# Kernel tuning notes

Hardware: AMD Instinct MI355X
Metric: run time of the kernel (lower is better)

The kernel has to match this reference:

```python
import jax, jax.numpy as jnp
import numpy as np

C = 256
CQK = C // 8


def setup_inputs() -> dict:
    key = jax.random.key(0)
    ks = jax.random.split(key, 8)
    B, H, W = 4, 64, 64
    x = jax.random.normal(ks[0], (B, C, H, W), dtype=jnp.float32)
    # 1x1 conv weights are plain [out_c, in_c] matrices + bias
    sq = 1.0 / np.sqrt(C)
    Wq = jax.random.uniform(ks[1], (CQK, C), jnp.float32, -sq, sq)
    bq = jax.random.uniform(ks[2], (CQK,), jnp.float32, -sq, sq)
    Wk = jax.random.uniform(ks[3], (CQK, C), jnp.float32, -sq, sq)
    bk = jax.random.uniform(ks[4], (CQK,), jnp.float32, -sq, sq)
    Wv = jax.random.uniform(ks[5], (C, C), jnp.float32, -sq, sq)
    bv = jax.random.uniform(ks[6], (C,), jnp.float32, -sq, sq)
    gamma = jnp.zeros((1,), dtype=jnp.float32)
    return {"x": x, "Wq": Wq, "bq": bq, "Wk": Wk, "bk": bk, "Wv": Wv, "bv": bv, "gamma": gamma}


def reference(x, Wq, bq, Wk, bk, Wv, bv, gamma):
    B, Cc, H, W = x.shape
    N = H * W
    xf = x.reshape(B, Cc, N)  # [B, C, N]
    # 1x1 convs == channel GEMMs
    q = jnp.einsum('dc,bcn->bdn', Wq, xf) + bq[None, :, None]  # [B, C/8, N]
    k = jnp.einsum('dc,bcn->bdn', Wk, xf) + bk[None, :, None]  # [B, C/8, N]
    v = jnp.einsum('dc,bcn->bdn', Wv, xf) + bv[None, :, None]  # [B, C, N]
    # attention[b, i, j] = softmax_j( q_i . k_j )  (no scaling, as in source)
    attn = jax.nn.softmax(jnp.einsum('bdn,bdm->bnm', q, k), axis=-1)  # [B, N, N]
    # out = value @ attention  (note: NOT attention^T, faithful to source)
    out = jnp.einsum('bcn,bnm->bcm', v, attn)  # [B, C, N]
    out = out.reshape(B, Cc, H, W)
    return gamma[0] * out + x
```

## Files before the change

### kernel.cpp

```cpp
#include <hip/hip_runtime.h>
#include <hip/hip_bf16.h>


#define NB 4
#define CC 256
#define NN 4096
#define L2E 1.44269504088896340f

typedef short  short4v  __attribute__((ext_vector_type(4)));
typedef short  short8v  __attribute__((ext_vector_type(8)));
typedef __bf16 bf16x8   __attribute__((ext_vector_type(8)));
typedef float  f32x4    __attribute__((ext_vector_type(4)));
typedef float  f32x16   __attribute__((ext_vector_type(16)));
typedef unsigned long u64x2 __attribute__((ext_vector_type(2)));
typedef unsigned int u32;

#define AS1 __attribute__((address_space(1)))
#define AS3 __attribute__((address_space(3)))

static __device__ __forceinline__ void gload16(const void* g, void* l) {
  __builtin_amdgcn_global_load_lds((const AS1 u32*)g, (AS3 u32*)l, 16, 0, 0);
}

static __device__ __forceinline__ unsigned short f2bf(float f) {
  union { __bf16 h; unsigned short u; } v; v.h = (__bf16)f; return v.u;
}
static __device__ __forceinline__ float bf2f(unsigned short u) {
  union { unsigned u; float f; } v; v.u = (u32)u << 16; return v.f;
}

union FragU { short8v s; bf16x8 b; unsigned u[4]; };

static __device__ __forceinline__ bf16x8 ld_frag(const unsigned short* p) {
  FragU u; u.s = *(const short8v*)p; return u.b;
}

static __device__ __forceinline__ f32x16 zero16() {
  f32x16 v;
#pragma unroll
  for (int i = 0; i < 16; ++i) v[i] = 0.0f;
  return v;
}

static __device__ __forceinline__ f32x16 mfma32(bf16x8 a, bf16x8 b, f32x16 c) {
  return __builtin_amdgcn_mfma_f32_32x32x16_bf16(a, b, c, 0, 0, 0);
}

__global__ __launch_bounds__(256) void k_wcvt(
    const float* __restrict__ Wq, const float* __restrict__ Wk,
    const float* __restrict__ Wv, unsigned short* __restrict__ Wb)
{
  const int i4 = blockIdx.x * 256 + threadIdx.x;
  const int e = i4 * 4;
  const int row = e >> 8, c = e & 255;
  const float* src = (row < 32) ? (Wq + row * 256 + c)
                   : (row < 64) ? (Wk + (row - 32) * 256 + c)
                                : (Wv + (row - 64) * 256 + c);
  f32x4 v = *(const f32x4*)src;
  short4v s;
#pragma unroll
  for (int j = 0; j < 4; ++j) s[j] = (short)f2bf(v[j]);
  *(short4v*)(Wb + e) = s;
}

__global__ __launch_bounds__(256) void k_proj(
    const float* __restrict__ x, const unsigned short* __restrict__ Wb,
    const float* __restrict__ bq, const float* __restrict__ bk,
    const float* __restrict__ bv,
    unsigned short* __restrict__ Qt, unsigned short* __restrict__ Kt,
    unsigned char* __restrict__ V8)
{
  __shared__ unsigned short xs[32][268];
  const int t = threadIdx.x;
  const int b = blockIdx.y;
  const int n0 = blockIdx.x * 32;
  const int w = t >> 6, l = t & 63, h = l >> 5, col = l & 31;

  const float* xb = x + (size_t)b * CC * NN;
  {
    const int c_off = t >> 3, nl = 4 * (t & 7);
#pragma unroll
    for (int c0 = 0; c0 < CC; c0 += 32) {
      int c = c0 + c_off;
      f32x4 v4 = *(const f32x4*)(xb + (size_t)c * NN + n0 + nl);
#pragma unroll
      for (int j = 0; j < 4; ++j) xs[nl + j][c] = f2bf(v4[j]);
    }
  }
  __syncthreads();

  for (int f = w; f < 10; f += 4) {
    const float* bsrc; int rowbase; int mode; int wrow;
    if (f == 0)      { bsrc = bq; rowbase = 0;            mode = 0; wrow = 0; }
    else if (f == 1) { bsrc = bk; rowbase = 0;            mode = 1; wrow = 32; }
    else             { bsrc = bv; rowbase = (f - 2) * 32; mode = 2; wrow = 64 + rowbase; }

    f32x16 acc0 = zero16();
    const unsigned short* wr = Wb + (size_t)(wrow + col) * 256 + 8 * h;

#pragma unroll
    for (int k0 = 0; k0 < CC; k0 += 16) {
      FragU a;
      a.s = *(const short8v*)(wr + k0);
      const unsigned short* p0 = &xs[col][k0 + 8 * h];
      FragU b0;
      short4v t0a = *(const short4v*)p0, t0b = *(const short4v*)(p0 + 4);
#pragma unroll
      for (int j = 0; j < 4; ++j) { b0.s[j] = t0a[j]; b0.s[4 + j] = t0b[j]; }
      acc0 = mfma32(a.b, b0.b, acc0);
    }

    const int n = n0 + col;
#pragma unroll
    for (int q = 0; q < 4; ++q) {
      f32x4 bias4 = *(const f32x4*)(bsrc + rowbase + 8 * q + 4 * h);
      float vals[4];
#pragma unroll
      for (int i = 0; i < 4; ++i) vals[i] = acc0[4 * q + i] + bias4[i];
      if (mode == 2) {
        const size_t tb = ((((size_t)b * 128 + (n >> 5)) * 2 + ((n >> 3) & 1)) * 256) * 16
                          + ((n >> 4) & 1) * 8 + (n & 7);
        u32 w01 = __builtin_amdgcn_cvt_pk_fp8_f32(vals[0], vals[1], 0, false);
        u32 w23 = __builtin_amdgcn_cvt_pk_fp8_f32(vals[2], vals[3], 0, false);
        const int cb0 = rowbase + 8 * q + 4 * h;
        V8[tb + (size_t)(cb0 + 0) * 16] = (unsigned char)(w01 & 0xff);
        V8[tb + (size_t)(cb0 + 1) * 16] = (unsigned char)((w01 >> 8) & 0xff);
        V8[tb + (size_t)(cb0 + 2) * 16] = (unsigned char)(w23 & 0xff);
        V8[tb + (size_t)(cb0 + 3) * 16] = (unsigned char)((w23 >> 8) & 0xff);
      } else {
        unsigned short* dst = (mode == 0) ? Qt : Kt;
        const float scale = (mode == 0) ? L2E : 1.0f;
        short4v s4;
#pragma unroll
        for (int i = 0; i < 4; ++i) s4[i] = (short)f2bf(vals[i] * scale);
        *(short4v*)(dst + ((size_t)b * NN + n) * 32 + 8 * q + 4 * h) = s4;
      }
    }
  }
}

__global__ __launch_bounds__(512) void k_rowstats(
    const unsigned short* __restrict__ Qt, const unsigned short* __restrict__ Kt,
    float* __restrict__ cbias)
{
  __shared__ float ssum[8][64];
  const int t = threadIdx.x;
  const int w = t >> 6, l = t & 63, h = l >> 5, col = l & 31;
  const int b = blockIdx.y;
  const int n0 = blockIdx.x * 64;
  const unsigned short* Qb = Qt + (size_t)b * NN * 32;
  const unsigned short* Kb = Kt + (size_t)b * NN * 32;

  bf16x8 bq00 = ld_frag(Qb + (size_t)(n0 + col) * 32 + 8 * h);
  bf16x8 bq01 = ld_frag(Qb + (size_t)(n0 + col) * 32 + 16 + 8 * h);
  bf16x8 bq10 = ld_frag(Qb + (size_t)(n0 + 32 + col) * 32 + 8 * h);
  bf16x8 bq11 = ld_frag(Qb + (size_t)(n0 + 32 + col) * 32 + 16 + 8 * h);

  float acc0 = 0.0f, acc1 = 0.0f;
  const int mbase = w * (NN / 8);
#pragma unroll 2
  for (int mt = 0; mt < 16; ++mt) {
    const int m0 = mbase + mt * 32;
    bf16x8 ak0 = ld_frag(Kb + (size_t)(m0 + col) * 32 + 8 * h);
    bf16x8 ak1 = ld_frag(Kb + (size_t)(m0 + col) * 32 + 16 + 8 * h);
    f32x16 S0 = zero16(), S1 = zero16();
    S0 = mfma32(ak0, bq00, S0);
    S0 = mfma32(ak1, bq01, S0);
    S1 = mfma32(ak0, bq10, S1);
    S1 = mfma32(ak1, bq11, S1);
    float p0 = 0.0f, p1 = 0.0f, p2 = 0.0f, p3 = 0.0f;
#pragma unroll
    for (int r = 0; r < 8; ++r) {
      p0 += __builtin_amdgcn_exp2f(S0[r]);
      p1 += __builtin_amdgcn_exp2f(S0[8 + r]);
      p2 += __builtin_amdgcn_exp2f(S1[r]);
      p3 += __builtin_amdgcn_exp2f(S1[8 + r]);
    }
    acc0 += p0 + p1;
    acc1 += p2 + p3;
  }
  acc0 += __shfl_xor(acc0, 32);
  acc1 += __shfl_xor(acc1, 32);

  if (l < 32) { ssum[w][l] = acc0; ssum[w][32 + l] = acc1; }
  __syncthreads();

  if (t < 64) {
    float s = 0.0f;
#pragma unroll
    for (int wv = 0; wv < 8; ++wv) s += ssum[wv][t];
    cbias[(size_t)b * NN + n0 + t] = -__builtin_amdgcn_logf(s);
  }
}

#define V_ISSUE(SET, TJ)                                                       \
  {                                                                            \
    const char* vg_ = vg + (size_t)(TJ) * 8192;                                \
    SET##A0 = *(const u64x2*)(vg_);                                            \
    SET##B0 = *(const u64x2*)(vg_ + 512);                                      \
    SET##A1 = *(const u64x2*)(vg_ + 8192);                                     \
    SET##B1 = *(const u64x2*)(vg_ + 8192 + 512);                               \
  }

#define PV_U(EBP, vA, vB)                                                      \
  {                                                                            \
    const char* eb_ = (EBP);                                                   \
    u64x2 ev0 = *(const u64x2*)(eb_);                                          \
    u64x2 ev1 = *(const u64x2*)(eb_ + 1024);                                   \
    u64x2 ev2 = *(const u64x2*)(eb_ + 2048);                                   \
    u64x2 ev3 = *(const u64x2*)(eb_ + 3072);                                   \
    long v00 = (long)vA[0], v10 = (long)vA[1];                                 \
    long v01 = (long)vB[0], v11 = (long)vB[1];                                 \
    acc[0][0] = __builtin_amdgcn_mfma_f32_32x32x16_fp8_fp8((long)ev0[0], v00, acc[0][0], 0, 0, 0); \
    acc[1][0] = __builtin_amdgcn_mfma_f32_32x32x16_fp8_fp8((long)ev1[0], v00, acc[1][0], 0, 0, 0); \
    acc[2][0] = __builtin_amdgcn_mfma_f32_32x32x16_fp8_fp8((long)ev2[0], v00, acc[2][0], 0, 0, 0); \
    acc[3][0] = __builtin_amdgcn_mfma_f32_32x32x16_fp8_fp8((long)ev3[0], v00, acc[3][0], 0, 0, 0); \
    acc[0][1] = __builtin_amdgcn_mfma_f32_32x32x16_fp8_fp8((long)ev0[0], v01, acc[0][1], 0, 0, 0); \
    acc[1][1] = __builtin_amdgcn_mfma_f32_32x32x16_fp8_fp8((long)ev1[0], v01, acc[1][1], 0, 0, 0); \
    acc[2][1] = __builtin_amdgcn_mfma_f32_32x32x16_fp8_fp8((long)ev2[0], v01, acc[2][1], 0, 0, 0); \
    acc[3][1] = __builtin_amdgcn_mfma_f32_32x32x16_fp8_fp8((long)ev3[0], v01, acc[3][1], 0, 0, 0); \
    acc[0][0] = __builtin_amdgcn_mfma_f32_32x32x16_fp8_fp8((long)ev0[1], v10, acc[0][0], 0, 0, 0); \
    acc[1][0] = __builtin_amdgcn_mfma_f32_32x32x16_fp8_fp8((long)ev1[1], v10, acc[1][0], 0, 0, 0); \
    acc[2][0] = __builtin_amdgcn_mfma_f32_32x32x16_fp8_fp8((long)ev2[1], v10, acc[2][0], 0, 0, 0); \
    acc[3][0] = __builtin_amdgcn_mfma_f32_32x32x16_fp8_fp8((long)ev3[1], v10, acc[3][0], 0, 0, 0); \
    acc[0][1] = __builtin_amdgcn_mfma_f32_32x32x16_fp8_fp8((long)ev0[1], v11, acc[0][1], 0, 0, 0); \
    acc[1][1] = __builtin_amdgcn_mfma_f32_32x32x16_fp8_fp8((long)ev1[1], v11, acc[1][1], 0, 0, 0); \
    acc[2][1] = __builtin_amdgcn_mfma_f32_32x32x16_fp8_fp8((long)ev2[1], v11, acc[2][1], 0, 0, 0); \
    acc[3][1] = __builtin_amdgcn_mfma_f32_32x32x16_fp8_fp8((long)ev3[1], v11, acc[3][1], 0, 0, 0); \
  }

#define K3_ITER(J, CUR, NXT)                                                   \
  if ((J) <= KJ) {                                                             \
    const int j_ = (J);                                                        \
    if (j_ + 1 < KJ) {                                                         \
      const size_t qoff_ = (size_t)(2 * j_ + 2) * 2048;                        \
      const int qs_ = (j_ + 1) & 1;                                            \
      if (ll == l) {                                                           \
        gload16(qsrc + qoff_, &qbuf[qs_][0][w * 256]);                         \
        gload16(qsrc + qoff_ + 2048, &qbuf[qs_][1][w * 256]);                  \
      }                                                                        \
    }                                                                          \
    if (w < 4) {                                                               \
      if (j_ < KJ) {                                                           \
        _Pragma("unroll")                                                      \
        for (int u = 0; u < 2; ++u) {                                          \
          const char* qb = &qbuf[j_ & 1][u][0];                                \
          FragU fq0, fq1;                                                      \
          fq0.s = *(const short8v*)(qb + l * 16);                              \
          fq1.s = *(const short8v*)(qb + 1024 + l * 16);                       \
          f32x16 S = zero16();                                                 \
          S = mfma32(fq0.b, bk0, S);                                           \
          S = mfma32(fq1.b, bk1, S);                                           \
          float e[16];                                                         \
          const float* cbi = cb + (2 * j_ + u) * 32;                           \
          _Pragma("unroll")                                                    \
          for (int q = 0; q < 4; ++q) {                                        \
            f32x4 cb4 = *(const f32x4*)(cbi + 8 * q + 4 * h);                  \
            _Pragma("unroll")                                                  \
            for (int i = 0; i < 4; ++i)                                        \
              e[4 * q + i] = __builtin_amdgcn_exp2f(S[4 * q + i] + cb4[i]);    \
          }                                                                    \
          u32 wA = __builtin_amdgcn_cvt_pk_fp8_f32(e[0], e[1], 0, false);      \
          wA = __builtin_amdgcn_cvt_pk_fp8_f32(e[2], e[3], wA, true);          \
          u32 wB = __builtin_amdgcn_cvt_pk_fp8_f32(e[4], e[5], 0, false);      \
          wB = __builtin_amdgcn_cvt_pk_fp8_f32(e[6], e[7], wB, true);          \
          u32 wC = __builtin_amdgcn_cvt_pk_fp8_f32(e[8], e[9], 0, false);      \
          wC = __builtin_amdgcn_cvt_pk_fp8_f32(e[10], e[11], wC, true);        \
          u32 wD = __builtin_amdgcn_cvt_pk_fp8_f32(e[12], e[13], 0, false);    \
          wD = __builtin_amdgcn_cvt_pk_fp8_f32(e[14], e[15], wD, true);        \
          asm("v_permlane32_swap_b32 %0, %1" : "+v"(wA), "+v"(wB));            \
          asm("v_permlane32_swap_b32 %0, %1" : "+v"(wC), "+v"(wD));            \
          u64x2 ev;                                                            \
          ev[0] = ((unsigned long)wB << 32) | wA;                              \
          ev[1] = ((unsigned long)wD << 32) | wC;                              \
          *(u64x2*)(&ebuf[j_ & 1][u][mfp * 1024 + l * 16]) = ev;               \
        }                                                                      \
      }                                                                        \
    } else {                                                                   \
      if (j_ < KJ) V_ISSUE(NXT, 2 * j_)                                        \
      if (j_ > 0) {                                                            \
        __builtin_amdgcn_s_setprio(1);                                         \
        PV_U(&ebuf[(j_ - 1) & 1][0][l * 16], CUR##A0, CUR##B0)                 \
        PV_U(&ebuf[(j_ - 1) & 1][1][l * 16], CUR##A1, CUR##B1)                 \
        __builtin_amdgcn_s_setprio(0);                                         \
      }                                                                        \
    }                                                                          \
    if (j_ < KJ) __syncthreads();                                              \
  }

__global__ __launch_bounds__(512) void k_attn_out(
    const unsigned short* __restrict__ Qt, const unsigned short* __restrict__ Kt,
    const unsigned char* __restrict__ V8,
    const float* __restrict__ cbias,
    unsigned short* __restrict__ pout,
    int nsplit, int nlen)
{
  __shared__ __align__(16) char qbuf[2][2][2048];
  __shared__ __align__(16) char ebuf[2][2][4096];

  const int wg = (int)blockIdx.x;
  const int chunk = (int)gridDim.x >> 3;
  const int id2 = (wg & 7) * chunk + (wg >> 3);
  const int per_b = 32 * nsplit;
  const int b = id2 / per_b;
  const int rem = id2 - b * per_b;
  const int ns = rem >> 5;
  const int m0 = (rem & 31) * 128;
  const int nbeg = ns * nlen;

  const int t = threadIdx.x;
  const int w = t >> 6, l = t & 63, h = l >> 5, col = l & 31;
  const int mfp = w & 3;
  const int ccons = (w & 3) * 64;

  const unsigned short* Kb = Kt + (size_t)b * NN * 32;
  const float* cb = cbias + (size_t)b * NN + nbeg;

  bf16x8 bk0 = ld_frag(Kb + (size_t)(m0 + 32 * mfp + col) * 32 + 8 * h);
  bf16x8 bk1 = ld_frag(Kb + (size_t)(m0 + 32 * mfp + col) * 32 + 16 + 8 * h);

  const int ll = l & 15;
  const size_t gqoff = (size_t)(((w & 1) * 16 + ll) * 64 + ((w >> 1) & 1) * 16
                                + (w >> 2) * 32);
  const char* qsrc = (const char*)Qt + ((size_t)b * NN + nbeg) * 64 + gqoff;

  const char* vg = (const char*)V8
      + (((size_t)b * 128 + (nbeg >> 5)) * 2 + h) * 4096
      + (size_t)(ccons + col) * 16;

  f32x16 acc[4][2];
#pragma unroll
  for (int mf = 0; mf < 4; ++mf)
#pragma unroll
    for (int cf = 0; cf < 2; ++cf) acc[mf][cf] = zero16();

  u64x2 S0A0, S0B0, S0A1, S0B1;
  u64x2 S1A0, S1B0, S1A1, S1B1;
  S0A0 = S0B0 = S0A1 = S0B1 = (u64x2)0;
  S1A0 = S1B0 = S1A1 = S1B1 = (u64x2)0;

  const int KJ = nlen >> 6;

  if (ll == l) {
    gload16(qsrc, &qbuf[0][0][w * 256]);
    gload16(qsrc + 2048, &qbuf[0][1][w * 256]);
  }
  __syncthreads();

  for (int jj = 0; jj <= KJ; jj += 2) {
    K3_ITER(jj,     S0, S1)
    K3_ITER(jj + 1, S1, S0)
  }

  if (w >= 4) {
    unsigned short* pb = pout + (((size_t)ns * NB + b) * NN + m0) * CC + ccons;
#pragma unroll
    for (int mf = 0; mf < 4; ++mf)
#pragma unroll
      for (int cf = 0; cf < 2; ++cf)
#pragma unroll
        for (int r = 0; r < 16; ++r) {
          int mloc = 32 * mf + (r & 3) + 8 * (r >> 2) + 4 * h;
          pb[(size_t)mloc * CC + 32 * cf + col] = f2bf(acc[mf][cf][r]);
        }
  }
}

__global__ __launch_bounds__(256) void k_comb(
    const unsigned short* __restrict__ pout, const float* __restrict__ x,
    const float* __restrict__ gamma, float* __restrict__ out, int nsplit)
{
  __shared__ float ld[64][65];
  const size_t STRIDE = (size_t)NB * CC * NN;
  const int t = threadIdx.x;
  const int m0 = blockIdx.x * 64, c0 = blockIdx.y * 64, b = blockIdx.z;
  const int ci = t & 63, mo = t >> 6;

  const unsigned short* pb = pout + ((size_t)b * NN + m0) * CC + c0;
#pragma unroll
  for (int rep = 0; rep < 16; ++rep) {
    const int mi = 4 * rep + mo;
    float s = bf2f(pb[(size_t)mi * CC + ci]);
    for (int ns = 1; ns < nsplit; ++ns)
      s += bf2f(pb[ns * STRIDE + (size_t)mi * CC + ci]);
    ld[mi][ci] = s;
  }
  __syncthreads();

  const float g = gamma[0];
  const int mi2 = t & 63;
#pragma unroll
  for (int rep = 0; rep < 16; ++rep) {
    const int cj = 4 * rep + mo;
    const size_t idx = ((size_t)b * CC + c0 + cj) * NN + m0 + mi2;
    out[idx] = g * ld[mi2][cj] + x[idx];
  }
}

extern "C" void kernel_launch(void* const* d_in, const int* in_sizes, int n_in,
                              void* d_out, int out_size, void* d_ws, size_t ws_size,
                              hipStream_t stream) {
  const float* x     = (const float*)d_in[0];
  const float* Wq    = (const float*)d_in[1];
  const float* bq    = (const float*)d_in[2];
  const float* Wk    = (const float*)d_in[3];
  const float* bk    = (const float*)d_in[4];
  const float* Wv    = (const float*)d_in[5];
  const float* bv    = (const float*)d_in[6];
  const float* gamma = (const float*)d_in[7];
  float* out = (float*)d_out;

  char* ws = (char*)d_ws;
  unsigned short* Qt = (unsigned short*)(ws);
  unsigned short* Kt = (unsigned short*)(ws + (1u << 20));
  unsigned char*  V8 = (unsigned char*)(ws + (2u << 20));
  unsigned short* Wb = (unsigned short*)(ws + (6u << 20));
  float* cbias = (float*)(ws + (10u << 20) + (2u << 18));
  const size_t POUT_OFF = (11u << 20);
  unsigned short* pout = (unsigned short*)(ws + POUT_OFF);
  const size_t PART_BYTES = (size_t)NB * CC * NN * 2;

  int nsplit = (ws_size >= POUT_OFF + 2 * PART_BYTES) ? 2 : 1;

  k_wcvt<<<dim3(80), 256, 0, stream>>>(Wq, Wk, Wv, Wb);
  k_proj<<<dim3(NN / 32, NB), 256, 0, stream>>>(x, Wb, bq, bk, bv, Qt, Kt, V8);
  k_rowstats<<<dim3(NN / 64, NB), 512, 0, stream>>>(Qt, Kt, cbias);
  k_attn_out<<<dim3(128 * nsplit), 512, 0, stream>>>(
      Qt, Kt, V8, cbias, pout, nsplit, NN / nsplit);
  k_comb<<<dim3(NN / 64, CC / 64, NB), 256, 0, stream>>>(pout, x, gamma, out, nsplit);
}
```

Baseline: 94.42 us.

## Replace producer/consumer wave split with uniform waves doing both QK and PV

The attention-output kernel previously split its 8 waves into 4 producers (QK^T, exp, fp8 pack into LDS) and 4 consumers (V loads plus PV MFMAs). Now every wave computes one 32x32 score tile and exp-packs it, then runs PV on 32 output channels with half the accumulators. Work is spread evenly and interleaved within each wave, so the exp/VALU phase and the MFMA phase can overlap across all waves instead of leaving half the waves idle in each phase. The cost is that each wave now loads twice as many E fragments from LDS per unit of PV work and holds both the QK and PV register state.

```diff
diff --git a/kernel.cpp b/kernel.cpp
--- a/kernel.cpp
+++ b/kernel.cpp
@@ -196,94 +196,96 @@
 #define V_ISSUE(SET, TJ)                                                       \
   {                                                                            \
     const char* vg_ = vg + (size_t)(TJ) * 8192;                                \
-    SET##A0 = *(const u64x2*)(vg_);                                            \
-    SET##B0 = *(const u64x2*)(vg_ + 512);                                      \
-    SET##A1 = *(const u64x2*)(vg_ + 8192);                                     \
-    SET##B1 = *(const u64x2*)(vg_ + 8192 + 512);                               \
-  }
-
-#define PV_U(EBP, vA, vB)                                                      \
+    SET##A = *(const u64x2*)(vg_);                                             \
+    SET##B = *(const u64x2*)(vg_ + 8192);                                      \
+  }
+
+#define PV_INT(EBSEL, vA, vB)                                                  \
   {                                                                            \
-    const char* eb_ = (EBP);                                                   \
-    u64x2 ev0 = *(const u64x2*)(eb_);                                          \
-    u64x2 ev1 = *(const u64x2*)(eb_ + 1024);                                   \
-    u64x2 ev2 = *(const u64x2*)(eb_ + 2048);                                   \
-    u64x2 ev3 = *(const u64x2*)(eb_ + 3072);                                   \
-    long v00 = (long)vA[0], v10 = (long)vA[1];                                 \
-    long v01 = (long)vB[0], v11 = (long)vB[1];                                 \
-    acc[0][0] = __builtin_amdgcn_mfma_f32_32x32x16_fp8_fp8((long)ev0[0], v00, acc[0][0], 0, 0, 0); \
-    acc[1][0] = __builtin_amdgcn_mfma_f32_32x32x16_fp8_fp8((long)ev1[0], v00, acc[1][0], 0, 0, 0); \
-    acc[2][0] = __builtin_amdgcn_mfma_f32_32x32x16_fp8_fp8((long)ev2[0], v00, acc[2][0], 0, 0, 0); \
-    acc[3][0] = __builtin_amdgcn_mfma_f32_32x32x16_fp8_fp8((long)ev3[0], v00, acc[3][0], 0, 0, 0); \
-    acc[0][1] = __builtin_amdgcn_mfma_f32_32x32x16_fp8_fp8((long)ev0[0], v01, acc[0][1], 0, 0, 0); \
-    acc[1][1] = __builtin_amdgcn_mfma_f32_32x32x16_fp8_fp8((long)ev1[0], v01, acc[1][1], 0, 0, 0); \
-    acc[2][1] = __builtin_amdgcn_mfma_f32_32x32x16_fp8_fp8((long)ev2[0], v01, acc[2][1], 0, 0, 0); \
-    acc[3][1] = __builtin_amdgcn_mfma_f32_32x32x16_fp8_fp8((long)ev3[0], v01, acc[3][1], 0, 0, 0); \
-    acc[0][0] = __builtin_amdgcn_mfma_f32_32x32x16_fp8_fp8((long)ev0[1], v10, acc[0][0], 0, 0, 0); \
-    acc[1][0] = __builtin_amdgcn_mfma_f32_32x32x16_fp8_fp8((long)ev1[1], v10, acc[1][0], 0, 0, 0); \
-    acc[2][0] = __builtin_amdgcn_mfma_f32_32x32x16_fp8_fp8((long)ev2[1], v10, acc[2][0], 0, 0, 0); \
-    acc[3][0] = __builtin_amdgcn_mfma_f32_32x32x16_fp8_fp8((long)ev3[1], v10, acc[3][0], 0, 0, 0); \
-    acc[0][1] = __builtin_amdgcn_mfma_f32_32x32x16_fp8_fp8((long)ev0[1], v11, acc[0][1], 0, 0, 0); \
-    acc[1][1] = __builtin_amdgcn_mfma_f32_32x32x16_fp8_fp8((long)ev1[1], v11, acc[1][1], 0, 0, 0); \
-    acc[2][1] = __builtin_amdgcn_mfma_f32_32x32x16_fp8_fp8((long)ev2[1], v11, acc[2][1], 0, 0, 0); \
-    acc[3][1] = __builtin_amdgcn_mfma_f32_32x32x16_fp8_fp8((long)ev3[1], v11, acc[3][1], 0, 0, 0); \
+    const char* eb0_ = &ebuf[EBSEL][0][l * 16];                                \
+    const char* eb1_ = &ebuf[EBSEL][1][l * 16];                                \
+    u64x2 e00 = *(const u64x2*)(eb0_);                                         \
+    u64x2 e01 = *(const u64x2*)(eb0_ + 1024);                                  \
+    u64x2 e02 = *(const u64x2*)(eb0_ + 2048);                                  \
+    u64x2 e03 = *(const u64x2*)(eb0_ + 3072);                                  \
+    u64x2 e10 = *(const u64x2*)(eb1_);                                         \
+    u64x2 e11 = *(const u64x2*)(eb1_ + 1024);                                  \
+    u64x2 e12 = *(const u64x2*)(eb1_ + 2048);                                  \
+    u64x2 e13 = *(const u64x2*)(eb1_ + 3072);                                  \
+    long va0 = (long)vA[0], va1 = (long)vA[1];                                 \
+    long vb0 = (long)vB[0], vb1 = (long)vB[1];                                 \
+    acc[0] = __builtin_amdgcn_mfma_f32_32x32x16_fp8_fp8((long)e00[0], va0, acc[0], 0, 0, 0); \
+    acc[1] = __builtin_amdgcn_mfma_f32_32x32x16_fp8_fp8((long)e01[0], va0, acc[1], 0, 0, 0); \
+    acc[2] = __builtin_amdgcn_mfma_f32_32x32x16_fp8_fp8((long)e02[0], va0, acc[2], 0, 0, 0); \
+    acc[3] = __builtin_amdgcn_mfma_f32_32x32x16_fp8_fp8((long)e03[0], va0, acc[3], 0, 0, 0); \
+    acc[0] = __builtin_amdgcn_mfma_f32_32x32x16_fp8_fp8((long)e00[1], va1, acc[0], 0, 0, 0); \
+    acc[1] = __builtin_amdgcn_mfma_f32_32x32x16_fp8_fp8((long)e01[1], va1, acc[1], 0, 0, 0); \
+    acc[2] = __builtin_amdgcn_mfma_f32_32x32x16_fp8_fp8((long)e02[1], va1, acc[2], 0, 0, 0); \
+    acc[3] = __builtin_amdgcn_mfma_f32_32x32x16_fp8_fp8((long)e03[1], va1, acc[3], 0, 0, 0); \
+    acc[0] = __builtin_amdgcn_mfma_f32_32x32x16_fp8_fp8((long)e10[0], vb0, acc[0], 0, 0, 0); \
+    acc[1] = __builtin_amdgcn_mfma_f32_32x32x16_fp8_fp8((long)e11[0], vb0, acc[1], 0, 0, 0); \
+    acc[2] = __builtin_amdgcn_mfma_f32_32x32x16_fp8_fp8((long)e12[0], vb0, acc[2], 0, 0, 0); \
+    acc[3] = __builtin_amdgcn_mfma_f32_32x32x16_fp8_fp8((long)e13[0], vb0, acc[3], 0, 0, 0); \
+    acc[0] = __builtin_amdgcn_mfma_f32_32x32x16_fp8_fp8((long)e10[1], vb1, acc[0], 0, 0, 0); \
+    acc[1] = __builtin_amdgcn_mfma_f32_32x32x16_fp8_fp8((long)e11[1], vb1, acc[1], 0, 0, 0); \
+    acc[2] = __builtin_amdgcn_mfma_f32_32x32x16_fp8_fp8((long)e12[1], vb1, acc[2], 0, 0, 0); \
+    acc[3] = __builtin_amdgcn_mfma_f32_32x32x16_fp8_fp8((long)e13[1], vb1, acc[3], 0, 0, 0); \
   }
 
 #define K3_ITER(J, CUR, NXT)                                                   \
   if ((J) <= KJ) {                                                             \
     const int j_ = (J);                                                        \
-    if (j_ + 1 < KJ) {                                                         \
+                                                             \
+    if (j_ + 1 < KJ && ll == l) {                                              \
       const size_t qoff_ = (size_t)(2 * j_ + 2) * 2048;                        \
       const int qs_ = (j_ + 1) & 1;                                            \
-      if (ll == l) {                                                           \
-        gload16(qsrc + qoff_, &qbuf[qs_][0][w * 256]);                         \
-        gload16(qsrc + qoff_ + 2048, &qbuf[qs_][1][w * 256]);                  \
+      gload16(qsrc + qoff_, &qbuf[qs_][0][w * 256]);                           \
+      gload16(qsrc + qoff_ + 2048, &qbuf[qs_][1][w * 256]);                    \
+    }                                                                          \
+                         \
+    if (j_ < KJ) V_ISSUE(NXT, 2 * j_)                                          \
+                                           \
+    f32x16 S;                                                                  \
+    if (j_ < KJ) {                                                             \
+      const char* qb = &qbuf[j_ & 1][up][0];                                   \
+      FragU fq0, fq1;                                                          \
+      fq0.s = *(const short8v*)(qb + l * 16);                                  \
+      fq1.s = *(const short8v*)(qb + 1024 + l * 16);                           \
+      S = zero16();                                                            \
+      S = mfma32(fq0.b, bk0, S);                                               \
+      S = mfma32(fq1.b, bk1, S);                                               \
+    }                                                                          \
+                                 \
+    if (j_ > 0) {                                                              \
+      __builtin_amdgcn_s_setprio(1);                                          \
+      PV_INT((j_ - 1) & 1, CUR##A, CUR##B)                                     \
+      __builtin_amdgcn_s_setprio(0);                                          \
+    }                                                                          \
+                                                       \
+    if (j_ < KJ) {                                                             \
+      float e[16];                                                             \
+      const float* cbi = cb + (2 * j_ + up) * 32;                              \
+      _Pragma("unroll")                                                        \
+      for (int q = 0; q < 4; ++q) {                                            \
+        f32x4 cb4 = *(const f32x4*)(cbi + 8 * q + 4 * h);                      \
+        _Pragma("unroll")                                                      \
+        for (int i = 0; i < 4; ++i)                                            \
+          e[4 * q + i] = __builtin_amdgcn_exp2f(S[4 * q + i] + cb4[i]);        \
       }                                                                        \
-    }                                                                          \
-    if (w < 4) {                                                               \
-      if (j_ < KJ) {                                                           \
-        _Pragma("unroll")                                                      \
-        for (int u = 0; u < 2; ++u) {                                          \
-          const char* qb = &qbuf[j_ & 1][u][0];                                \
-          FragU fq0, fq1;                                                      \
-          fq0.s = *(const short8v*)(qb + l * 16);                              \
-          fq1.s = *(const short8v*)(qb + 1024 + l * 16);                       \
-          f32x16 S = zero16();                                                 \
-          S = mfma32(fq0.b, bk0, S);                                           \
-          S = mfma32(fq1.b, bk1, S);                                           \
-          float e[16];                                                         \
-          const float* cbi = cb + (2 * j_ + u) * 32;                           \
-          _Pragma("unroll")                                                    \
-          for (int q = 0; q < 4; ++q) {                                        \
-            f32x4 cb4 = *(const f32x4*)(cbi + 8 * q + 4 * h);                  \
-            _Pragma("unroll")                                                  \
-            for (int i = 0; i < 4; ++i)                                        \
-              e[4 * q + i] = __builtin_amdgcn_exp2f(S[4 * q + i] + cb4[i]);    \
-          }                                                                    \
-          u32 wA = __builtin_amdgcn_cvt_pk_fp8_f32(e[0], e[1], 0, false);      \
-          wA = __builtin_amdgcn_cvt_pk_fp8_f32(e[2], e[3], wA, true);          \
-          u32 wB = __builtin_amdgcn_cvt_pk_fp8_f32(e[4], e[5], 0, false);      \
-          wB = __builtin_amdgcn_cvt_pk_fp8_f32(e[6], e[7], wB, true);          \
-          u32 wC = __builtin_amdgcn_cvt_pk_fp8_f32(e[8], e[9], 0, false);      \
-          wC = __builtin_amdgcn_cvt_pk_fp8_f32(e[10], e[11], wC, true);        \
-          u32 wD = __builtin_amdgcn_cvt_pk_fp8_f32(e[12], e[13], 0, false);    \
-          wD = __builtin_amdgcn_cvt_pk_fp8_f32(e[14], e[15], wD, true);        \
-          asm("v_permlane32_swap_b32 %0, %1" : "+v"(wA), "+v"(wB));            \
-          asm("v_permlane32_swap_b32 %0, %1" : "+v"(wC), "+v"(wD));            \
-          u64x2 ev;                                                            \
-          ev[0] = ((unsigned long)wB << 32) | wA;                              \
-          ev[1] = ((unsigned long)wD << 32) | wC;                              \
-          *(u64x2*)(&ebuf[j_ & 1][u][mfp * 1024 + l * 16]) = ev;               \
-        }                                                                      \
-      }                                                                        \
-    } else {                                                                   \
-      if (j_ < KJ) V_ISSUE(NXT, 2 * j_)                                        \
-      if (j_ > 0) {                                                            \
-        __builtin_amdgcn_s_setprio(1);                                         \
-        PV_U(&ebuf[(j_ - 1) & 1][0][l * 16], CUR##A0, CUR##B0)                 \
-        PV_U(&ebuf[(j_ - 1) & 1][1][l * 16], CUR##A1, CUR##B1)                 \
-        __builtin_amdgcn_s_setprio(0);                                         \
-      }                                                                        \
+      u32 wA = __builtin_amdgcn_cvt_pk_fp8_f32(e[0], e[1], 0, false);          \
+      wA = __builtin_amdgcn_cvt_pk_fp8_f32(e[2], e[3], wA, true);              \
+      u32 wB = __builtin_amdgcn_cvt_pk_fp8_f32(e[4], e[5], 0, false);          \
+      wB = __builtin_amdgcn_cvt_pk_fp8_f32(e[6], e[7], wB, true);              \
+      u32 wC = __builtin_amdgcn_cvt_pk_fp8_f32(e[8], e[9], 0, false);          \
+      wC = __builtin_amdgcn_cvt_pk_fp8_f32(e[10], e[11], wC, true);            \
+      u32 wD = __builtin_amdgcn_cvt_pk_fp8_f32(e[12], e[13], 0, false);        \
+      wD = __builtin_amdgcn_cvt_pk_fp8_f32(e[14], e[15], wD, true);            \
+      asm("v_permlane32_swap_b32 %0, %1" : "+v"(wA), "+v"(wB));                \
+      asm("v_permlane32_swap_b32 %0, %1" : "+v"(wC), "+v"(wD));                \
+      u64x2 ev;                                                                \
+      ev[0] = ((unsigned long)wB << 32) | wA;                                  \
+      ev[1] = ((unsigned long)wD << 32) | wC;                                  \
+      *(u64x2*)(&ebuf[j_ & 1][up][mfp * 1024 + l * 16]) = ev;                  \
     }                                                                          \
     if (j_ < KJ) __syncthreads();                                              \
   }
@@ -310,8 +312,9 @@
 
   const int t = threadIdx.x;
   const int w = t >> 6, l = t & 63, h = l >> 5, col = l & 31;
-  const int mfp = w & 3;
-  const int ccons = (w & 3) * 64;
+  const int up = w & 1;
+  const int mfp = w >> 1;
+  const int ccons = w * 32;
 
   const unsigned short* Kb = Kt + (size_t)b * NN * 32;
   const float* cb = cbias + (size_t)b * NN + nbeg;
@@ -328,16 +331,12 @@
       + (((size_t)b * 128 + (nbeg >> 5)) * 2 + h) * 4096
       + (size_t)(ccons + col) * 16;
 
-  f32x16 acc[4][2];
-#pragma unroll
-  for (int mf = 0; mf < 4; ++mf)
-#pragma unroll
-    for (int cf = 0; cf < 2; ++cf) acc[mf][cf] = zero16();
-
-  u64x2 S0A0, S0B0, S0A1, S0B1;
-  u64x2 S1A0, S1B0, S1A1, S1B1;
-  S0A0 = S0B0 = S0A1 = S0B1 = (u64x2)0;
-  S1A0 = S1B0 = S1A1 = S1B1 = (u64x2)0;
+  f32x16 acc[4];
+#pragma unroll
+  for (int mf = 0; mf < 4; ++mf) acc[mf] = zero16();
+
+  u64x2 S0A, S0B, S1A, S1B;
+  S0A = S0B = S1A = S1B = (u64x2)0;
 
   const int KJ = nlen >> 6;
 
@@ -352,17 +351,15 @@
     K3_ITER(jj + 1, S1, S0)
   }
 
-  if (w >= 4) {
+  {
     unsigned short* pb = pout + (((size_t)ns * NB + b) * NN + m0) * CC + ccons;
 #pragma unroll
     for (int mf = 0; mf < 4; ++mf)
 #pragma unroll
-      for (int cf = 0; cf < 2; ++cf)
-#pragma unroll
-        for (int r = 0; r < 16; ++r) {
-          int mloc = 32 * mf + (r & 3) + 8 * (r >> 2) + 4 * h;
-          pb[(size_t)mloc * CC + 32 * cf + col] = f2bf(acc[mf][cf][r]);
-        }
+      for (int r = 0; r < 16; ++r) {
+        int mloc = 32 * mf + (r & 3) + 8 * (r >> 2) + 4 * h;
+        pb[(size_t)mloc * CC + col] = f2bf(acc[mf][r]);
+      }
   }
 }
 
```

Result: slower. 98.07 us (+3.9%).

## Materialize fp8 attention matrix in global memory, split into emat and PV kernels

Applied to the files above, without the earlier changes.

Replaces the fused attention-output kernel, which recomputed exponentials in LDS with producer/consumer warps and split-N partial outputs, with two kernels. The first writes the full fp8 exp-matrix E to global memory, and the second runs the PV GEMM and fuses the gamma*out + x epilogue, so the partial-sum combine kernel goes away. The aim is simpler, fully parallel stages without intra-block syncs or split reductions. In exchange it writes and reads a 64MB fp8 matrix (4x4096x4096 bytes) through HBM, which adds substantial memory traffic.

```diff
diff --git a/kernel.cpp b/kernel.cpp
--- a/kernel.cpp
+++ b/kernel.cpp
@@ -15,13 +15,6 @@
 typedef unsigned long u64x2 __attribute__((ext_vector_type(2)));
 typedef unsigned int u32;
 
-#define AS1 __attribute__((address_space(1)))
-#define AS3 __attribute__((address_space(3)))
-
-static __device__ __forceinline__ void gload16(const void* g, void* l) {
-  __builtin_amdgcn_global_load_lds((const AS1 u32*)g, (AS3 u32*)l, 16, 0, 0);
-}
-
 static __device__ __forceinline__ unsigned short f2bf(float f) {
   union { __bf16 h; unsigned short u; } v; v.h = (__bf16)f; return v.u;
 }
@@ -44,6 +37,9 @@
 
 static __device__ __forceinline__ f32x16 mfma32(bf16x8 a, bf16x8 b, f32x16 c) {
   return __builtin_amdgcn_mfma_f32_32x32x16_bf16(a, b, c, 0, 0, 0);
+}
+static __device__ __forceinline__ f32x16 mfma8(long a, long b, f32x16 c) {
+  return __builtin_amdgcn_mfma_f32_32x32x16_fp8_fp8(a, b, c, 0, 0, 0);
 }
 
 __global__ __launch_bounds__(256) void k_wcvt(
@@ -193,207 +189,117 @@
   }
 }
 
-#define V_ISSUE(SET, TJ)                                                       \
-  {                                                                            \
-    const char* vg_ = vg + (size_t)(TJ) * 8192;                                \
-    SET##A0 = *(const u64x2*)(vg_);                                            \
-    SET##B0 = *(const u64x2*)(vg_ + 512);                                      \
-    SET##A1 = *(const u64x2*)(vg_ + 8192);                                     \
-    SET##B1 = *(const u64x2*)(vg_ + 8192 + 512);                               \
-  }
-
-#define PV_U(EBP, vA, vB)                                                      \
-  {                                                                            \
-    const char* eb_ = (EBP);                                                   \
-    u64x2 ev0 = *(const u64x2*)(eb_);                                          \
-    u64x2 ev1 = *(const u64x2*)(eb_ + 1024);                                   \
-    u64x2 ev2 = *(const u64x2*)(eb_ + 2048);                                   \
-    u64x2 ev3 = *(const u64x2*)(eb_ + 3072);                                   \
-    long v00 = (long)vA[0], v10 = (long)vA[1];                                 \
-    long v01 = (long)vB[0], v11 = (long)vB[1];                                 \
-    acc[0][0] = __builtin_amdgcn_mfma_f32_32x32x16_fp8_fp8((long)ev0[0], v00, acc[0][0], 0, 0, 0); \
-    acc[1][0] = __builtin_amdgcn_mfma_f32_32x32x16_fp8_fp8((long)ev1[0], v00, acc[1][0], 0, 0, 0); \
-    acc[2][0] = __builtin_amdgcn_mfma_f32_32x32x16_fp8_fp8((long)ev2[0], v00, acc[2][0], 0, 0, 0); \
-    acc[3][0] = __builtin_amdgcn_mfma_f32_32x32x16_fp8_fp8((long)ev3[0], v00, acc[3][0], 0, 0, 0); \
-    acc[0][1] = __builtin_amdgcn_mfma_f32_32x32x16_fp8_fp8((long)ev0[0], v01, acc[0][1], 0, 0, 0); \
-    acc[1][1] = __builtin_amdgcn_mfma_f32_32x32x16_fp8_fp8((long)ev1[0], v01, acc[1][1], 0, 0, 0); \
-    acc[2][1] = __builtin_amdgcn_mfma_f32_32x32x16_fp8_fp8((long)ev2[0], v01, acc[2][1], 0, 0, 0); \
-    acc[3][1] = __builtin_amdgcn_mfma_f32_32x32x16_fp8_fp8((long)ev3[0], v01, acc[3][1], 0, 0, 0); \
-    acc[0][0] = __builtin_amdgcn_mfma_f32_32x32x16_fp8_fp8((long)ev0[1], v10, acc[0][0], 0, 0, 0); \
-    acc[1][0] = __builtin_amdgcn_mfma_f32_32x32x16_fp8_fp8((long)ev1[1], v10, acc[1][0], 0, 0, 0); \
-    acc[2][0] = __builtin_amdgcn_mfma_f32_32x32x16_fp8_fp8((long)ev2[1], v10, acc[2][0], 0, 0, 0); \
-    acc[3][0] = __builtin_amdgcn_mfma_f32_32x32x16_fp8_fp8((long)ev3[1], v10, acc[3][0], 0, 0, 0); \
-    acc[0][1] = __builtin_amdgcn_mfma_f32_32x32x16_fp8_fp8((long)ev0[1], v11, acc[0][1], 0, 0, 0); \
-    acc[1][1] = __builtin_amdgcn_mfma_f32_32x32x16_fp8_fp8((long)ev1[1], v11, acc[1][1], 0, 0, 0); \
-    acc[2][1] = __builtin_amdgcn_mfma_f32_32x32x16_fp8_fp8((long)ev2[1], v11, acc[2][1], 0, 0, 0); \
-    acc[3][1] = __builtin_amdgcn_mfma_f32_32x32x16_fp8_fp8((long)ev3[1], v11, acc[3][1], 0, 0, 0); \
-  }
-
-#define K3_ITER(J, CUR, NXT)                                                   \
-  if ((J) <= KJ) {                                                             \
-    const int j_ = (J);                                                        \
-    if (j_ + 1 < KJ) {                                                         \
-      const size_t qoff_ = (size_t)(2 * j_ + 2) * 2048;                        \
-      const int qs_ = (j_ + 1) & 1;                                            \
-      if (ll == l) {                                                           \
-        gload16(qsrc + qoff_, &qbuf[qs_][0][w * 256]);                         \
-        gload16(qsrc + qoff_ + 2048, &qbuf[qs_][1][w * 256]);                  \
-      }                                                                        \
-    }                                                                          \
-    if (w < 4) {                                                               \
-      if (j_ < KJ) {                                                           \
-        _Pragma("unroll")                                                      \
-        for (int u = 0; u < 2; ++u) {                                          \
-          const char* qb = &qbuf[j_ & 1][u][0];                                \
-          FragU fq0, fq1;                                                      \
-          fq0.s = *(const short8v*)(qb + l * 16);                              \
-          fq1.s = *(const short8v*)(qb + 1024 + l * 16);                       \
-          f32x16 S = zero16();                                                 \
-          S = mfma32(fq0.b, bk0, S);                                           \
-          S = mfma32(fq1.b, bk1, S);                                           \
-          float e[16];                                                         \
-          const float* cbi = cb + (2 * j_ + u) * 32;                           \
-          _Pragma("unroll")                                                    \
-          for (int q = 0; q < 4; ++q) {                                        \
-            f32x4 cb4 = *(const f32x4*)(cbi + 8 * q + 4 * h);                  \
-            _Pragma("unroll")                                                  \
-            for (int i = 0; i < 4; ++i)                                        \
-              e[4 * q + i] = __builtin_amdgcn_exp2f(S[4 * q + i] + cb4[i]);    \
-          }                                                                    \
-          u32 wA = __builtin_amdgcn_cvt_pk_fp8_f32(e[0], e[1], 0, false);      \
-          wA = __builtin_amdgcn_cvt_pk_fp8_f32(e[2], e[3], wA, true);          \
-          u32 wB = __builtin_amdgcn_cvt_pk_fp8_f32(e[4], e[5], 0, false);      \
-          wB = __builtin_amdgcn_cvt_pk_fp8_f32(e[6], e[7], wB, true);          \
-          u32 wC = __builtin_amdgcn_cvt_pk_fp8_f32(e[8], e[9], 0, false);      \
-          wC = __builtin_amdgcn_cvt_pk_fp8_f32(e[10], e[11], wC, true);        \
-          u32 wD = __builtin_amdgcn_cvt_pk_fp8_f32(e[12], e[13], 0, false);    \
-          wD = __builtin_amdgcn_cvt_pk_fp8_f32(e[14], e[15], wD, true);        \
-          asm("v_permlane32_swap_b32 %0, %1" : "+v"(wA), "+v"(wB));            \
-          asm("v_permlane32_swap_b32 %0, %1" : "+v"(wC), "+v"(wD));            \
-          u64x2 ev;                                                            \
-          ev[0] = ((unsigned long)wB << 32) | wA;                              \
-          ev[1] = ((unsigned long)wD << 32) | wC;                              \
-          *(u64x2*)(&ebuf[j_ & 1][u][mfp * 1024 + l * 16]) = ev;               \
-        }                                                                      \
-      }                                                                        \
-    } else {                                                                   \
-      if (j_ < KJ) V_ISSUE(NXT, 2 * j_)                                        \
-      if (j_ > 0) {                                                            \
-        __builtin_amdgcn_s_setprio(1);                                         \
-        PV_U(&ebuf[(j_ - 1) & 1][0][l * 16], CUR##A0, CUR##B0)                 \
-        PV_U(&ebuf[(j_ - 1) & 1][1][l * 16], CUR##A1, CUR##B1)                 \
-        __builtin_amdgcn_s_setprio(0);                                         \
-      }                                                                        \
-    }                                                                          \
-    if (j_ < KJ) __syncthreads();                                              \
-  }
-
-__global__ __launch_bounds__(512) void k_attn_out(
+__global__ __launch_bounds__(512) void k_emat(
     const unsigned short* __restrict__ Qt, const unsigned short* __restrict__ Kt,
-    const unsigned char* __restrict__ V8,
-    const float* __restrict__ cbias,
-    unsigned short* __restrict__ pout,
-    int nsplit, int nlen)
-{
-  __shared__ __align__(16) char qbuf[2][2][2048];
-  __shared__ __align__(16) char ebuf[2][2][4096];
-
-  const int wg = (int)blockIdx.x;
-  const int chunk = (int)gridDim.x >> 3;
-  const int id2 = (wg & 7) * chunk + (wg >> 3);
-  const int per_b = 32 * nsplit;
-  const int b = id2 / per_b;
-  const int rem = id2 - b * per_b;
-  const int ns = rem >> 5;
-  const int m0 = (rem & 31) * 128;
-  const int nbeg = ns * nlen;
-
+    const float* __restrict__ cbias, unsigned char* __restrict__ E8)
+{
   const int t = threadIdx.x;
   const int w = t >> 6, l = t & 63, h = l >> 5, col = l & 31;
-  const int mfp = w & 3;
-  const int ccons = (w & 3) * 64;
-
+  const int b = blockIdx.y;
+  const int n0 = blockIdx.x * 32;
+  const unsigned short* Qb = Qt + (size_t)b * NN * 32;
   const unsigned short* Kb = Kt + (size_t)b * NN * 32;
-  const float* cb = cbias + (size_t)b * NN + nbeg;
-
-  bf16x8 bk0 = ld_frag(Kb + (size_t)(m0 + 32 * mfp + col) * 32 + 8 * h);
-  bf16x8 bk1 = ld_frag(Kb + (size_t)(m0 + 32 * mfp + col) * 32 + 16 + 8 * h);
-
-  const int ll = l & 15;
-  const size_t gqoff = (size_t)(((w & 1) * 16 + ll) * 64 + ((w >> 1) & 1) * 16
-                                + (w >> 2) * 32);
-  const char* qsrc = (const char*)Qt + ((size_t)b * NN + nbeg) * 64 + gqoff;
-
-  const char* vg = (const char*)V8
-      + (((size_t)b * 128 + (nbeg >> 5)) * 2 + h) * 4096
-      + (size_t)(ccons + col) * 16;
-
-  f32x16 acc[4][2];
-#pragma unroll
-  for (int mf = 0; mf < 4; ++mf)
-#pragma unroll
-    for (int cf = 0; cf < 2; ++cf) acc[mf][cf] = zero16();
-
-  u64x2 S0A0, S0B0, S0A1, S0B1;
-  u64x2 S1A0, S1B0, S1A1, S1B1;
-  S0A0 = S0B0 = S0A1 = S0B1 = (u64x2)0;
-  S1A0 = S1B0 = S1A1 = S1B1 = (u64x2)0;
-
-  const int KJ = nlen >> 6;
-
-  if (ll == l) {
-    gload16(qsrc, &qbuf[0][0][w * 256]);
-    gload16(qsrc + 2048, &qbuf[0][1][w * 256]);
-  }
+
+  bf16x8 aq0 = ld_frag(Qb + (size_t)(n0 + col) * 32 + 8 * h);
+  bf16x8 aq1 = ld_frag(Qb + (size_t)(n0 + col) * 32 + 16 + 8 * h);
+
+  f32x4 cb4[4];
+  const float* cbi = cbias + (size_t)b * NN + n0;
+#pragma unroll
+  for (int q = 0; q < 4; ++q) cb4[q] = *(const f32x4*)(cbi + 8 * q + 4 * h);
+
+  unsigned char* st = E8 + ((size_t)b * 512 + 2 * (size_t)(n0 >> 4) + h) * 32768;
+
+#pragma unroll 2
+  for (int mt = 0; mt < 16; ++mt) {
+    const int m0 = w * 512 + mt * 32;
+    bf16x8 bk0 = ld_frag(Kb + (size_t)(m0 + col) * 32 + 8 * h);
+    bf16x8 bk1 = ld_frag(Kb + (size_t)(m0 + col) * 32 + 16 + 8 * h);
+    f32x16 S = zero16();
+    S = mfma32(aq0, bk0, S);
+    S = mfma32(aq1, bk1, S);
+
+    float e[16];
+#pragma unroll
+    for (int q = 0; q < 4; ++q)
+#pragma unroll
+      for (int i = 0; i < 4; ++i)
+        e[4 * q + i] = __builtin_amdgcn_exp2f(S[4 * q + i] + cb4[q][i]);
+
+    u32 wA = __builtin_amdgcn_cvt_pk_fp8_f32(e[0], e[1], 0, false);
+    wA = __builtin_amdgcn_cvt_pk_fp8_f32(e[2], e[3], wA, true);
+    u32 wB = __builtin_amdgcn_cvt_pk_fp8_f32(e[4], e[5], 0, false);
+    wB = __builtin_amdgcn_cvt_pk_fp8_f32(e[6], e[7], wB, true);
+    u32 wC = __builtin_amdgcn_cvt_pk_fp8_f32(e[8], e[9], 0, false);
+    wC = __builtin_amdgcn_cvt_pk_fp8_f32(e[10], e[11], wC, true);
+    u32 wD = __builtin_amdgcn_cvt_pk_fp8_f32(e[12], e[13], 0, false);
+    wD = __builtin_amdgcn_cvt_pk_fp8_f32(e[14], e[15], wD, true);
+    asm("v_permlane32_swap_b32 %0, %1" : "+v"(wA), "+v"(wB));
+    asm("v_permlane32_swap_b32 %0, %1" : "+v"(wC), "+v"(wD));
+    unsigned long ev0 = ((unsigned long)wB << 32) | wA;
+    unsigned long ev1 = ((unsigned long)wD << 32) | wC;
+
+    *(unsigned long*)(st + (size_t)(m0 + col) * 8) = ev0;
+    *(unsigned long*)(st + 65536 + (size_t)(m0 + col) * 8) = ev1;
+  }
+}
+
+__global__ __launch_bounds__(512) void k_pv(
+    const unsigned char* __restrict__ E8, const unsigned char* __restrict__ V8,
+    const float* __restrict__ x, const float* __restrict__ gamma,
+    float* __restrict__ out)
+{
+  __shared__ unsigned short ldb[64][264];
+  const int t = threadIdx.x;
+  const int w = t >> 6, l = t & 63, h = l >> 5, col = l & 31;
+  const int b = blockIdx.y;
+  const int m0 = blockIdx.x * 64;
+  const int mf = w & 1, cc = (w >> 1) * 64;
+
+  const unsigned char* ep = E8 + ((size_t)b * 512 + h) * 32768
+                            + (size_t)(m0 + mf * 32 + col) * 8;
+  const unsigned char* vp = V8 + ((size_t)b * 256 + h) * 4096
+                            + (size_t)(cc + col) * 16;
+
+  f32x16 acc[2];
+  acc[0] = zero16();
+  acc[1] = zero16();
+
+#pragma unroll 4
+  for (int nt = 0; nt < 128; ++nt) {
+    unsigned long e0 = *(const unsigned long*)(ep);
+    unsigned long e1 = *(const unsigned long*)(ep + 65536);
+    u64x2 vA = *(const u64x2*)(vp);
+    u64x2 vB = *(const u64x2*)(vp + 512);
+    acc[0] = mfma8((long)e0, (long)vA[0], acc[0]);
+    acc[1] = mfma8((long)e0, (long)vB[0], acc[1]);
+    acc[0] = mfma8((long)e1, (long)vA[1], acc[0]);
+    acc[1] = mfma8((long)e1, (long)vB[1], acc[1]);
+    ep += 131072;
+    vp += 8192;
+  }
+
+#pragma unroll
+  for (int cf = 0; cf < 2; ++cf)
+#pragma unroll
+    for (int r = 0; r < 16; ++r) {
+      int mloc = mf * 32 + (r & 3) + 8 * (r >> 2) + 4 * h;
+      ldb[mloc][cc + 32 * cf + col] = f2bf(acc[cf][r]);
+    }
   __syncthreads();
 
-  for (int jj = 0; jj <= KJ; jj += 2) {
-    K3_ITER(jj,     S0, S1)
-    K3_ITER(jj + 1, S1, S0)
-  }
-
-  if (w >= 4) {
-    unsigned short* pb = pout + (((size_t)ns * NB + b) * NN + m0) * CC + ccons;
-#pragma unroll
-    for (int mf = 0; mf < 4; ++mf)
-#pragma unroll
-      for (int cf = 0; cf < 2; ++cf)
-#pragma unroll
-        for (int r = 0; r < 16; ++r) {
-          int mloc = 32 * mf + (r & 3) + 8 * (r >> 2) + 4 * h;
-          pb[(size_t)mloc * CC + 32 * cf + col] = f2bf(acc[mf][cf][r]);
-        }
-  }
-}
-
-__global__ __launch_bounds__(256) void k_comb(
-    const unsigned short* __restrict__ pout, const float* __restrict__ x,
-    const float* __restrict__ gamma, float* __restrict__ out, int nsplit)
-{
-  __shared__ float ld[64][65];
-  const size_t STRIDE = (size_t)NB * CC * NN;
-  const int t = threadIdx.x;
-  const int m0 = blockIdx.x * 64, c0 = blockIdx.y * 64, b = blockIdx.z;
-  const int ci = t & 63, mo = t >> 6;
-
-  const unsigned short* pb = pout + ((size_t)b * NN + m0) * CC + c0;
-#pragma unroll
-  for (int rep = 0; rep < 16; ++rep) {
-    const int mi = 4 * rep + mo;
-    float s = bf2f(pb[(size_t)mi * CC + ci]);
-    for (int ns = 1; ns < nsplit; ++ns)
-      s += bf2f(pb[ns * STRIDE + (size_t)mi * CC + ci]);
-    ld[mi][ci] = s;
-  }
-  __syncthreads();
-
   const float g = gamma[0];
-  const int mi2 = t & 63;
-#pragma unroll
-  for (int rep = 0; rep < 16; ++rep) {
-    const int cj = 4 * rep + mo;
-    const size_t idx = ((size_t)b * CC + c0 + cj) * NN + m0 + mi2;
-    out[idx] = g * ld[mi2][cj] + x[idx];
+  const int ci = t >> 4;
+  const int m4 = (t & 15) * 4;
+#pragma unroll
+  for (int rnd = 0; rnd < 8; ++rnd) {
+    const int c = 32 * rnd + ci;
+    const size_t idx = ((size_t)b * CC + c) * NN + m0 + m4;
+    f32x4 xv = *(const f32x4*)(x + idx);
+    f32x4 o;
+#pragma unroll
+    for (int k = 0; k < 4; ++k) o[k] = g * bf2f(ldb[m4 + k][c]) + xv[k];
+    *(f32x4*)(out + idx) = o;
   }
 }
 
@@ -415,17 +321,12 @@
   unsigned short* Kt = (unsigned short*)(ws + (1u << 20));
   unsigned char*  V8 = (unsigned char*)(ws + (2u << 20));
   unsigned short* Wb = (unsigned short*)(ws + (6u << 20));
-  float* cbias = (float*)(ws + (10u << 20) + (2u << 18));
-  const size_t POUT_OFF = (11u << 20);
-  unsigned short* pout = (unsigned short*)(ws + POUT_OFF);
-  const size_t PART_BYTES = (size_t)NB * CC * NN * 2;
-
-  int nsplit = (ws_size >= POUT_OFF + 2 * PART_BYTES) ? 2 : 1;
+  float* cbias = (float*)(ws + (6u << 20) + (1u << 18));
+  unsigned char* E8  = (unsigned char*)(ws + (7u << 20));
 
   k_wcvt<<<dim3(80), 256, 0, stream>>>(Wq, Wk, Wv, Wb);
   k_proj<<<dim3(NN / 32, NB), 256, 0, stream>>>(x, Wb, bq, bk, bv, Qt, Kt, V8);
   k_rowstats<<<dim3(NN / 64, NB), 512, 0, stream>>>(Qt, Kt, cbias);
-  k_attn_out<<<dim3(128 * nsplit), 512, 0, stream>>>(
-      Qt, Kt, V8, cbias, pout, nsplit, NN / nsplit);
-  k_comb<<<dim3(NN / 64, CC / 64, NB), 256, 0, stream>>>(pout, x, gamma, out, nsplit);
-}
+  k_emat<<<dim3(NN / 32, NB), 512, 0, stream>>>(Qt, Kt, cbias, E8);
+  k_pv<<<dim3(NN / 64, NB), 512, 0, stream>>>(E8, V8, x, gamma, out);
+}
```

Result: slower. 100.0 us (+5.9%).
